# Optimization experiments

Measured on AMD Instinct MI355X. Metric: run time of the kernel, lower is better.

Reference implementation:

```python
import jax, jax.numpy as jnp
import numpy as np

COV_LOSS_WT = 1.0


def setup_inputs() -> dict:
    key = jax.random.key(0)
    ks = jax.random.split(key, 6)
    B, T, S, H = 8, 64, 256, 768
    sc = 1.0 / np.sqrt(H)
    return {
        "decoder_outputs": jax.random.normal(ks[0], (B, T, H), jnp.float32),
        "decoder_input_mask": jnp.ones((B, T), jnp.float32),
        "encoder_outputs": jax.random.normal(ks[1], (B, S, H), jnp.float32),
        "enc_padding_mask": jnp.ones((B, S), jnp.float32),
        "coverage": jnp.zeros((B, S), jnp.float32),
        "W_h": (jax.random.normal(ks[2], (H, H), jnp.float32) * sc),
        "W_dec": (jax.random.normal(ks[3], (H, H), jnp.float32) * sc),
        "b_dec": jnp.zeros((H,), jnp.float32),
        "w_c": (jax.random.normal(ks[4], (H,), jnp.float32) * sc),
        "v": (jax.random.normal(ks[5], (H,), jnp.float32) * sc),
    }


def reference(decoder_outputs, decoder_input_mask, encoder_outputs,
              enc_padding_mask, coverage, W_h, W_dec, b_dec, w_c, v):
    # Precompute projections (same math as expanding att_features then adding
    # the coverage feature per step).
    enc_feature = encoder_outputs @ W_h.T                 # [B,S,H]
    dec_fea = decoder_outputs @ W_dec.T + b_dec           # [B,T,H]

    def step(cov, dec_t):
        # cov: [B,S], dec_t: [B,H]
        e = jnp.tanh(enc_feature + dec_t[:, None, :] + cov[:, :, None] * w_c)  # [B,S,H]
        scores = e @ v                                    # [B,S]
        attn = jax.nn.softmax(scores, axis=-1) * enc_padding_mask
        attn = attn / attn.sum(-1, keepdims=True)
        ht = jnp.einsum('bs,bsh->bh', attn, encoder_outputs)
        step_loss = COV_LOSS_WT * jnp.sum(jnp.minimum(attn, cov), axis=-1)     # [B]
        return cov + attn, (ht, attn, step_loss)

    coverage_final, (ht, attn, step_losses) = jax.lax.scan(
        step, coverage, jnp.swapaxes(dec_fea, 0, 1))      # scan over T

    ht_hat = jnp.swapaxes(ht, 0, 1)                       # [B,T,H]
    attn_dist = jnp.swapaxes(attn, 0, 1)                  # [B,T,S]
    converge_loss = jnp.sum(step_losses * decoder_input_mask.T) / jnp.sum(decoder_input_mask)
    return (ht_hat, attn_dist, converge_loss, coverage_final)
```

## Files before the change

kernel.cpp:

```cpp
#include <hip/hip_runtime.h>

#define Bq 8
#define Tq 64
#define Sq 256
#define Hq 768
#define TT 8
#define ST 16

typedef float f32x4 __attribute__((ext_vector_type(4)));
typedef __bf16 bf16x8 __attribute__((ext_vector_type(8)));

#define TANH_SCALE 2.885390081777927f
#define LOG2E 1.4426950408889634f

template <int Ctrl, int Rmask>
__device__ __forceinline__ float dpp_add_f(float v) {
  int t = __builtin_amdgcn_update_dpp(0, __float_as_int(v), Ctrl, Rmask, 0xF, true);
  return v + __int_as_float(t);
}
__device__ __forceinline__ float wave64_sum(float v) {
  v = dpp_add_f<0xB1, 0xF>(v);
  v = dpp_add_f<0x4E, 0xF>(v);
  v = dpp_add_f<0x141, 0xF>(v);
  v = dpp_add_f<0x140, 0xF>(v);
  v = dpp_add_f<0x142, 0xA>(v);
  v = dpp_add_f<0x143, 0xC>(v);
  return __int_as_float(__builtin_amdgcn_readlane(__float_as_int(v), 63));
}

__device__ __forceinline__ uint2 cvt4(f32x4 v) {
  union { __bf16 h[4]; uint2 u; } t;
  t.h[0] = (__bf16)v[0]; t.h[1] = (__bf16)v[1];
  t.h[2] = (__bf16)v[2]; t.h[3] = (__bf16)v[3];
  return t.u;
}

__global__ __launch_bounds__(256, 4) void proj_kernel(
    const float* __restrict__ enc, const float* __restrict__ dec,
    const float* __restrict__ Wh, const float* __restrict__ Wd,
    const float* __restrict__ bd,
    const float* __restrict__ wcvec, const float* __restrict__ vvec,
    __bf16* __restrict__ efh, __bf16* __restrict__ decfh,
    float* __restrict__ w1g, float* __restrict__ lacc,
    unsigned* __restrict__ cnt)
{
  {
    int gidx = blockIdx.x * 256 + threadIdx.x;
    if (gidx < Hq) w1g[gidx] = vvec[gidx] * wcvec[gidx];
    if (gidx < 64) cnt[gidx] = 0u;
    if (gidx == 0) lacc[0] = 0.f;
  }

  __shared__ unsigned short As[2][32][40];
  __shared__ unsigned short Bs[2][64][40];

  int bid = blockIdx.x;
  const float* A; const float* W; bool isEf;
  int bm, bn;
  if (bid < 768) {
    A = enc; W = Wh; isEf = true;
    bm = bid % 64; bn = bid / 64;
  } else {
    bid -= 768;
    A = dec; W = Wd; isEf = false;
    bm = bid % 16; bn = bid / 16;
  }
  const int m0 = bm * 32, n0 = bn * 64;

  const int ti = threadIdx.x;
  const int rowA = ti >> 3, colA = (ti & 7) * 4;
  const int rowB = ti >> 2, colB = (ti & 3) * 8;
  const float* pa = A + (size_t)(m0 + rowA) * Hq + colA;
  const float* pw = W + (size_t)(n0 + rowB) * Hq + colB;

  {
    f32x4 a0 = *(const f32x4*)pa;
    f32x4 w0 = *(const f32x4*)pw, w1 = *(const f32x4*)(pw + 4);
    *(uint2*)&As[0][rowA][colA]     = cvt4(a0);
    *(uint2*)&Bs[0][rowB][colB]     = cvt4(w0);
    *(uint2*)&Bs[0][rowB][colB + 4] = cvt4(w1);
  }
  __syncthreads();

  const int w = ti >> 6, ln = ti & 63;
  const int mh = (w >> 1) * 16, nh = (w & 1) * 32;
  const int rsel = ln & 15, kofe = (ln >> 4) * 8;

  f32x4 acc[2] = {};
  for (int k = 0; k < 24; k++) {
    f32x4 na, nw0, nw1;
    if (k < 23) {
      na  = *(const f32x4*)(pa + (k + 1) * 32);
      nw0 = *(const f32x4*)(pw + (k + 1) * 32);
      nw1 = *(const f32x4*)(pw + (k + 1) * 32 + 4);
    }
    const int cur = k & 1;
    bf16x8 af = *(const bf16x8*)&As[cur][mh + rsel][kofe];
    bf16x8 b0 = *(const bf16x8*)&Bs[cur][nh + rsel][kofe];
    bf16x8 b1 = *(const bf16x8*)&Bs[cur][nh + 16 + rsel][kofe];
    acc[0] = __builtin_amdgcn_mfma_f32_16x16x32_bf16(af, b0, acc[0], 0, 0, 0);
    acc[1] = __builtin_amdgcn_mfma_f32_16x16x32_bf16(af, b1, acc[1], 0, 0, 0);
    if (k < 23) {
      const int nxt = cur ^ 1;
      *(uint2*)&As[nxt][rowA][colA]     = cvt4(na);
      *(uint2*)&Bs[nxt][rowB][colB]     = cvt4(nw0);
      *(uint2*)&Bs[nxt][rowB][colB + 4] = cvt4(nw1);
      __syncthreads();
    }
  }

  const int col = ln & 15, rb = (ln >> 4) * 4;
#pragma unroll
  for (int tn = 0; tn < 2; tn++)
#pragma unroll
    for (int j = 0; j < 4; j++) {
      int r = m0 + mh + rb + j, c = n0 + nh + tn * 16 + col;
      float val = acc[tn][j];
      if (isEf) {
        efh[(size_t)r * Hq + c] =
            (__bf16)__builtin_amdgcn_exp2f(val * TANH_SCALE);
      } else {
        decfh[(size_t)r * Hq + c] =
            (__bf16)__builtin_amdgcn_exp2f((val + bd[c]) * TANH_SCALE);
      }
    }
}

__global__ __launch_bounds__(256, 4) void abscan_kernel(
    const __bf16* __restrict__ efh, const __bf16* __restrict__ decfh,
    const float* __restrict__ vvec, const float* __restrict__ w1g,
    const float* __restrict__ emask, const float* __restrict__ cov0,
    const float* __restrict__ dmask,
    float2* __restrict__ ab,
    float* __restrict__ out_attn, float* __restrict__ out_covf,
    float* __restrict__ lacc, unsigned* __restrict__ cnt)
{
  __shared__ double smem_raw[4808];
  const int bid = blockIdx.x;
  const int tid = threadIdx.x;

  if (bid < 1024) {
    unsigned short (*efs)[780] = (unsigned short(*)[780])smem_raw;
    unsigned short (*dts)[776] = (unsigned short(*)[776])((char*)smem_raw + 24960);
    float (*part)[2]           = (float(*)[2])((char*)smem_raw + 37376);
    const int b = bid & 7;
    const int r = bid >> 3;
    const int kchunk = r & 7;
    const int tt0 = kchunk * TT;
    const int st0 = (r >> 3) * ST;

    for (int i = tid; i < ST * 192; i += 256) {
      int row = i / 192, c = (i % 192) * 4;
      *(uint2*)&efs[row][c] =
          *(const uint2*)(efh + (size_t)(b * Sq + st0 + row) * Hq + c);
    }
    for (int i = tid; i < TT * 192; i += 256) {
      int row = i / 192, c = (i % 192) * 4;
      *(uint2*)&dts[row][c] =
          *(const uint2*)(decfh + (size_t)(b * Tq + tt0 + row) * Hq + c);
    }
    __syncthreads();

    const int hh = tid >> 7;
    const int pid = tid & 127;
    const int tl = pid >> 4, sl = pid & 15;
    const int hbase = hh * 384;
    const int hbu = __builtin_amdgcn_readfirstlane(hbase);
    const float* vp  = vvec + hbu;
    const float* w1p = w1g + hbu;

    float A = 0.f, B = 0.f;
#define BLO(x) __uint_as_float((x) << 16)
#define BHI(x) __uint_as_float((x) & 0xFFFF0000u)
#pragma unroll 4
    for (int j = 0; j < 384; j += 4) {
      uint2 eu = *(const uint2*)&efs[sl][hbase + j];
      uint2 du = *(const uint2*)&dts[tl][hbase + j];
      f32x4 v4 = *(const f32x4*)(vp + j);
      f32x4 w1 = *(const f32x4*)(w1p + j);
      float e2[4];
      e2[0] = BLO(eu.x) * BLO(du.x);
      e2[1] = BHI(eu.x) * BHI(du.x);
      e2[2] = BLO(eu.y) * BLO(du.y);
      e2[3] = BHI(eu.y) * BHI(du.y);
#pragma unroll
      for (int e = 0; e < 4; e++) {
        float rr = __builtin_amdgcn_rcpf(1.f + e2[e]);
        float t0 = 1.f - 2.f * rr;
        float f1 = 1.f - t0 * t0;
        A += v4[e] * t0;
        B += w1[e] * f1;
      }
    }
#undef BLO
#undef BHI

    if (hh == 1) { part[pid][0] = A; part[pid][1] = B; }
    __syncthreads();
    if (hh == 0) {
      union { float2 f; unsigned long long u; } cv;
      cv.f.x = A + part[pid][0];
      cv.f.y = B + part[pid][1];
      __hip_atomic_store(
          (unsigned long long*)&ab[(size_t)(b * Tq + tt0 + tl) * Sq + st0 + sl],
          cv.u, __ATOMIC_RELAXED, __HIP_MEMORY_SCOPE_AGENT);
    }
    __syncthreads();
    if (tid == 0)
      __hip_atomic_fetch_add(&cnt[b * 8 + kchunk], 1u,
                             __ATOMIC_RELAXED, __HIP_MEMORY_SCOPE_AGENT);
  } else {
    float* zp   = (float*)smem_raw;
    float* dms  = (float*)smem_raw + 8;
    float* lred = (float*)smem_raw + 72;
    const int b = bid - 1024;
    const int s = tid, w = tid >> 6, ln = tid & 63;
    if (tid < Tq) dms[tid] = dmask[b * Tq + tid];
    const float em = emask[b * Sq + s];
    float cov = cov0[b * Sq + s];
    float lp = 0.f;
    const unsigned long long* P =
        (const unsigned long long*)(ab + (size_t)b * Tq * Sq + s);

    for (int kc = 0; kc < 8; kc++) {
      if (tid == 0)
        while (__hip_atomic_load(&cnt[b * 8 + kc],
                                 __ATOMIC_RELAXED, __HIP_MEMORY_SCOPE_AGENT) < 16u)
          __builtin_amdgcn_s_sleep(2);
      __syncthreads();

      union { unsigned long long u; float2 f; } cv[8];
#pragma unroll
      for (int j = 0; j < 8; j++)
        cv[j].u = __hip_atomic_load(P + (size_t)(kc * 8 + j) * Sq,
                                    __ATOMIC_RELAXED, __HIP_MEMORY_SCOPE_AGENT);

#pragma unroll
      for (int j = 0; j < 8; j++) {
        const int t = kc * 8 + j;
        float sc = cv[j].f.x + cov * cv[j].f.y;
        float E = __builtin_amdgcn_exp2f(sc * LOG2E) * em;
        float wsum = wave64_sum(E);
        if (ln == 0) zp[(t & 1) * 4 + w] = wsum;
        __syncthreads();
        float Z = zp[(t & 1) * 4 + 0] + zp[(t & 1) * 4 + 1] +
                  zp[(t & 1) * 4 + 2] + zp[(t & 1) * 4 + 3];
        float at = E * __builtin_amdgcn_rcpf(Z);
        lp += fminf(at, cov) * dms[t];
        cov += at;
        out_attn[(size_t)(b * Tq + t) * Sq + s] = at;
      }
    }

    out_covf[b * Sq + s] = cov;
    float wl = wave64_sum(lp);
    if (ln == 0) lred[w] = wl;
    __syncthreads();
    if (tid == 0) atomicAdd(lacc, lred[0] + lred[1] + lred[2] + lred[3]);
  }
}

__global__ __launch_bounds__(256) void ht_kernel(
    const float* __restrict__ attn, const float* __restrict__ enc,
    const float* __restrict__ dmask, const float* __restrict__ lacc,
    float* __restrict__ out_ht, float* __restrict__ out_loss)
{
  __shared__ float lat[Sq][8];
  __shared__ float r4[4];
  int bid = blockIdx.x;
  int b = bid / 24, r = bid % 24, tc = r / 3, hc = r % 3;
  int tid = threadIdx.x;
  int h = hc * 256 + tid;
#pragma unroll
  for (int tt = 0; tt < 8; tt++)
    lat[tid][tt] = attn[(size_t)(b * Tq + tc * 8 + tt) * Sq + tid];
  __syncthreads();

  float acc[8] = {};
  const float* ep = enc + (size_t)(b * Sq) * Hq + h;
  for (int sb = 0; sb < Sq; sb += 8) {
    float e[8];
#pragma unroll
    for (int u = 0; u < 8; u++) e[u] = ep[(size_t)(sb + u) * Hq];
#pragma unroll
    for (int u = 0; u < 8; u++) {
      f32x4 a0 = *(const f32x4*)&lat[sb + u][0];
      f32x4 a1 = *(const f32x4*)&lat[sb + u][4];
      acc[0] += a0[0] * e[u]; acc[1] += a0[1] * e[u];
      acc[2] += a0[2] * e[u]; acc[3] += a0[3] * e[u];
      acc[4] += a1[0] * e[u]; acc[5] += a1[1] * e[u];
      acc[6] += a1[2] * e[u]; acc[7] += a1[3] * e[u];
    }
  }
#pragma unroll
  for (int tt = 0; tt < 8; tt++)
    out_ht[(size_t)(b * Tq + tc * 8 + tt) * Hq + h] = acc[tt];

  if (blockIdx.x == 0) {
    float s = 0.f;
    for (int i = tid; i < Bq * Tq; i += 256) s += dmask[i];
#pragma unroll
    for (int off = 32; off; off >>= 1) s += __shfl_xor(s, off);
    int w = tid >> 6, ln = tid & 63;
    if (ln == 0) r4[w] = s;
    __syncthreads();
    if (tid == 0) out_loss[0] = lacc[0] / (r4[0] + r4[1] + r4[2] + r4[3]);
  }
}

extern "C" void kernel_launch(void* const* d_in, const int* in_sizes, int n_in,
                              void* d_out, int out_size, void* d_ws, size_t ws_size,
                              hipStream_t stream) {
  const float* dec   = (const float*)d_in[0];
  const float* dmask = (const float*)d_in[1];
  const float* enc   = (const float*)d_in[2];
  const float* emask = (const float*)d_in[3];
  const float* cov0  = (const float*)d_in[4];
  const float* Wh    = (const float*)d_in[5];
  const float* Wd    = (const float*)d_in[6];
  const float* bd    = (const float*)d_in[7];
  const float* wc    = (const float*)d_in[8];
  const float* vv    = (const float*)d_in[9];
  float* out = (float*)d_out;

  char* ws = (char*)d_ws;
  __bf16*   efh   = (__bf16*)ws;
  __bf16*   decfh = (__bf16*)(ws + 3145728);
  float2*   ab    = (float2*)(ws + 3932160);
  float*    w1g   = (float*)(ws + 4980736);
  float*    lacc  = (float*)(ws + 4983808);
  unsigned* cnt   = (unsigned*)(ws + 4983872);

  const size_t OFF_ATTN = (size_t)Bq * Tq * Hq;
  const size_t OFF_LOSS = OFF_ATTN + (size_t)Bq * Tq * Sq;
  const size_t OFF_COV  = OFF_LOSS + 1;

  proj_kernel<<<960, 256, 0, stream>>>(enc, dec, Wh, Wd, bd, wc, vv,
                                       efh, decfh, w1g, lacc, cnt);
  abscan_kernel<<<1032, 256, 0, stream>>>(efh, decfh, vv, w1g, emask, cov0,
                                          dmask, ab,
                                          out + OFF_ATTN, out + OFF_COV,
                                          lacc, cnt);
  ht_kernel<<<192, 256, 0, stream>>>(out + OFF_ATTN, enc, dmask, lacc,
                                     out, out + OFF_LOSS);
}
```

Baseline: 84.94 us.

## Run coverage scan in a single wave to drop per-step block barriers

The sequential coverage/softmax scan block now uses only one 64-lane wave, with each lane handling four sequence positions. The per-step softmax normaliser comes from a DPP wave reduction instead of shared memory plus __syncthreads, and the spin-wait on producer counters runs wave-wide with readfirstlane instead of a barrier. Score loads are software-pipelined two steps ahead. This is meant to shorten the serial critical path of the 64-step scan, at the cost of less parallelism per step.

```diff
diff --git a/kernel.cpp b/kernel.cpp
--- a/kernel.cpp
+++ b/kernel.cpp
@@ -210,53 +210,74 @@
       __hip_atomic_fetch_add(&cnt[b * 8 + kchunk], 1u,
                              __ATOMIC_RELAXED, __HIP_MEMORY_SCOPE_AGENT);
   } else {
-    float* zp   = (float*)smem_raw;
-    float* dms  = (float*)smem_raw + 8;
-    float* lred = (float*)smem_raw + 72;
+    if (tid >= 64) return;
     const int b = bid - 1024;
-    const int s = tid, w = tid >> 6, ln = tid & 63;
-    if (tid < Tq) dms[tid] = dmask[b * Tq + tid];
-    const float em = emask[b * Sq + s];
-    float cov = cov0[b * Sq + s];
+    const int ln = tid;
+    float dm = dmask[b * Tq + ln];
+    float cov[4], em[4], E[4];
     float lp = 0.f;
+#pragma unroll
+    for (int i = 0; i < 4; i++) {
+      cov[i] = cov0[b * Sq + ln + 64 * i];
+      em[i]  = emask[b * Sq + ln + 64 * i];
+    }
     const unsigned long long* P =
-        (const unsigned long long*)(ab + (size_t)b * Tq * Sq + s);
+        (const unsigned long long*)(ab + (size_t)b * Tq * Sq + ln);
+    union U64 { unsigned long long u; float2 f; };
+    U64 cv0[4], cv1[4];
 
     for (int kc = 0; kc < 8; kc++) {
-      if (tid == 0)
-        while (__hip_atomic_load(&cnt[b * 8 + kc],
-                                 __ATOMIC_RELAXED, __HIP_MEMORY_SCOPE_AGENT) < 16u)
-          __builtin_amdgcn_s_sleep(2);
-      __syncthreads();
-
-      union { unsigned long long u; float2 f; } cv[8];
-#pragma unroll
-      for (int j = 0; j < 8; j++)
-        cv[j].u = __hip_atomic_load(P + (size_t)(kc * 8 + j) * Sq,
-                                    __ATOMIC_RELAXED, __HIP_MEMORY_SCOPE_AGENT);
+      unsigned c;
+      do {
+        c = __hip_atomic_load(&cnt[b * 8 + kc],
+                              __ATOMIC_RELAXED, __HIP_MEMORY_SCOPE_AGENT);
+      } while (__builtin_amdgcn_readfirstlane(c) < 16u);
+
+      const int tb = kc * 8;
+#pragma unroll
+      for (int i = 0; i < 4; i++)
+        cv0[i].u = __hip_atomic_load(P + (size_t)tb * Sq + 64 * i,
+                                     __ATOMIC_RELAXED, __HIP_MEMORY_SCOPE_AGENT);
+#pragma unroll
+      for (int i = 0; i < 4; i++)
+        cv1[i].u = __hip_atomic_load(P + (size_t)(tb + 1) * Sq + 64 * i,
+                                     __ATOMIC_RELAXED, __HIP_MEMORY_SCOPE_AGENT);
 
 #pragma unroll
       for (int j = 0; j < 8; j++) {
-        const int t = kc * 8 + j;
-        float sc = cv[j].f.x + cov * cv[j].f.y;
-        float E = __builtin_amdgcn_exp2f(sc * LOG2E) * em;
-        float wsum = wave64_sum(E);
-        if (ln == 0) zp[(t & 1) * 4 + w] = wsum;
-        __syncthreads();
-        float Z = zp[(t & 1) * 4 + 0] + zp[(t & 1) * 4 + 1] +
-                  zp[(t & 1) * 4 + 2] + zp[(t & 1) * 4 + 3];
-        float at = E * __builtin_amdgcn_rcpf(Z);
-        lp += fminf(at, cov) * dms[t];
-        cov += at;
-        out_attn[(size_t)(b * Tq + t) * Sq + s] = at;
+        const int t = tb + j;
+        float s4 = 0.f;
+#pragma unroll
+        for (int i = 0; i < 4; i++) {
+          float sc = cv0[i].f.x + cov[i] * cv0[i].f.y;
+          E[i] = __builtin_amdgcn_exp2f(sc * LOG2E) * em[i];
+          s4 += E[i];
+        }
+#pragma unroll
+        for (int i = 0; i < 4; i++) {
+          cv0[i] = cv1[i];
+          if (j < 6)
+            cv1[i].u = __hip_atomic_load(P + (size_t)(t + 2) * Sq + 64 * i,
+                                         __ATOMIC_RELAXED, __HIP_MEMORY_SCOPE_AGENT);
+        }
+        float Z = wave64_sum(s4);
+        float invZ = __builtin_amdgcn_rcpf(Z);
+        float dmt = __shfl(dm, t);
+#pragma unroll
+        for (int i = 0; i < 4; i++) {
+          float at = E[i] * invZ;
+          lp += fminf(at, cov[i]) * dmt;
+          cov[i] += at;
+          out_attn[(size_t)(b * Tq + t) * Sq + ln + 64 * i] = at;
+        }
       }
     }
 
-    out_covf[b * Sq + s] = cov;
+#pragma unroll
+    for (int i = 0; i < 4; i++)
+      out_covf[b * Sq + ln + 64 * i] = cov[i];
     float wl = wave64_sum(lp);
-    if (ln == 0) lred[w] = wl;
-    __syncthreads();
-    if (tid == 0) atomicAdd(lacc, lred[0] + lred[1] + lred[2] + lred[3]);
+    if (ln == 0) atomicAdd(lacc, wl);
   }
 }
 
```

After: 80.25 us. -5.5%, faster.
